# Kernel optimization log

Measured on AMD Instinct MI355X. Metric: run time of the kernel, lower is better.

## Reference

```python
import jax, jax.numpy as jnp
from jax import lax
import numpy as np

VTH = 0.2
DECAY = 0.25            # LIF membrane decay used by pcdmd slayers.LIFSpike (STBP-style)
DT = 0.001              # norse default integration step
TAU_SYN_INV = 200.0     # norse LSNNParameters defaults
TAU_MEM_INV = 100.0
TAU_ADAPT_INV = 1.0 / 700.0
BETA = 0.0              # module sets beta=0 (no threshold adaptation jumps)
ALPHA = 100.0           # SuperSpike surrogate slope (norse 'super' method)

@jax.custom_vjp
def spike_rect(v):
    # Heaviside forward, rectangular surrogate backward (STBP)
    return (v > 0).astype(v.dtype)

def _sr_fwd(v):
    return spike_rect(v), v

def _sr_bwd(v, g):
    return (g * (jnp.abs(v) < 0.5).astype(g.dtype),)

spike_rect.defvjp(_sr_fwd, _sr_bwd)

@jax.custom_vjp
def spike_super(v):
    # Heaviside forward, SuperSpike surrogate backward (norse 'super')
    return (v > 0).astype(v.dtype)

def _ss_fwd(v):
    return spike_super(v), v

def _ss_bwd(v, g):
    return (g / (ALPHA * jnp.abs(v) + 1.0) ** 2,)

spike_super.defvjp(_ss_fwd, _ss_bwd)

def lif_spike(x):
    # x: [..., T] -> spike train [..., T]
    # u_t = DECAY * u_{t-1} * (1 - o_{t-1}) + x_t ; o_t = H(u_t - VTH)
    xT = jnp.moveaxis(x, -1, 0)  # [T, ...]
    u0 = jnp.zeros(xT.shape[1:], x.dtype)
    def step(carry, xt):
        u, o = carry
        u = DECAY * u * (1.0 - o) + xt
        o = spike_rect(u - VTH)
        return (u, o), o
    _, out = lax.scan(step, (u0, u0), xT)
    return jnp.moveaxis(out, 0, -1)

def lsnn_recurrent(x, w_in, w_rec):
    # x: [T, B, H] input spikes; norse LSNNRecurrent lsnn_step with beta=0, v_th=VTH
    x_in = jnp.einsum('tbh,oh->tbo', x, w_in)  # input current, hoisted out of scan
    B, H = x.shape[1], w_in.shape[0]
    z0 = jnp.zeros((B, H), x.dtype)
    state0 = (z0, z0, z0, jnp.full((B, H), VTH, x.dtype))  # z, v, i, b (b starts at v_th)
    def step(state, xt):
        z, v, i, b = state
        i_jump = i + xt + z @ w_rec.T
        v_dec = v + DT * TAU_MEM_INV * (-v + i_jump)          # v_leak = 0
        i_dec = i_jump - DT * TAU_SYN_INV * i_jump
        b_dec = b + DT * TAU_ADAPT_INV * (VTH - b)
        z_new = spike_super(v_dec - b_dec)
        v_new = (1.0 - z_new) * v_dec                          # v_reset = 0
        b_new = b_dec + z_new * TAU_ADAPT_INV * BETA
        return (z_new, v_new, i_dec, b_new), z_new
    _, out = lax.scan(step, state0, x_in)
    return out  # [T, B, H]

def setup_inputs() -> dict:
    key = jax.random.key(0)
    ks = jax.random.split(key, 7)
    B, T = 64, 8192
    EEG_C, AUD_C, H, OUT = 64, 1, 10, 2
    x = jax.random.normal(ks[0], (B, 1, EEG_C + 2 * AUD_C, T), jnp.float32)
    s_in = 1.0 / float(np.sqrt(EEG_C))
    s_h = 1.0 / float(np.sqrt(H))
    return {
        'x': x,
        'w_front': jax.random.uniform(ks[1], (H, EEG_C), jnp.float32, -s_in, s_in),
        'b_front': jax.random.uniform(ks[2], (H,), jnp.float32, -s_in, s_in),
        'w_in': jax.random.uniform(ks[3], (H, H), jnp.float32, -s_h, s_h),
        'w_rec': jax.random.uniform(ks[4], (H, H), jnp.float32, -s_h, s_h),
        'w_cls': jax.random.uniform(ks[5], (OUT, H), jnp.float32, -s_h, s_h),
        'b_cls': jax.random.uniform(ks[6], (OUT,), jnp.float32, -s_h, s_h),
    }

def reference(x, w_front, b_front, w_in, w_rec, w_cls, b_cls):
    AUD_C = 1
    window_length = x.shape[-1]
    eeg = x[:, 0, AUD_C:-AUD_C, :]                              # [B, 64, T]
    eeg = jnp.einsum('bct,hc->bht', eeg, w_front) + b_front[None, :, None]
    eeg = lif_spike(eeg)                                        # spike_tanh in snn mode
    eeg = jnp.transpose(eeg, (2, 0, 1))                         # [T, B, H]
    z = lsnn_recurrent(eeg, w_in, w_rec)                        # [T, B, H]
    out = jnp.transpose(z, (1, 2, 0))                           # [B, H, T]
    out = jnp.einsum('bht,oh->bot', out, w_cls) + b_cls[None, :, None]
    out = lif_spike(out)                                        # spike_sigmoid in snn mode
    return jnp.sum(out, axis=2) / window_length                 # [B, 2]
```

## Files before the change

### kernel.cpp

```cpp
#include <hip/hip_runtime.h>
#include <cstdint>
#include <cstddef>

#define T_LEN 8192
#define BATCH 64
#define HID   10
#define CH    66
#define EEG   64
#define SM_STRIDE 8384
#define TS    1060

__global__ __launch_bounds__(256) void k_front_lif(
    const float* __restrict__ x, const float* __restrict__ wf_g,
    const float* __restrict__ bf_g, unsigned short* __restrict__ smask,
    float* __restrict__ out) {
    __shared__ float wf[EEG][HID];
    __shared__ float bf[HID];
    __shared__ float yt[HID][TS];
    int tid = threadIdx.x;
    for (int i = tid; i < EEG * HID; i += 256) {
        int h = i / EEG, c = i % EEG;
        wf[c][h] = wf_g[i];
    }
    if (tid < HID) bf[tid] = bf_g[tid];

    int chunk = blockIdx.x;
    int b     = blockIdx.y;
    if (chunk == 0) {
        for (int i = tid; i < 96; i += 256)
            ((unsigned*)(smask + (size_t)b * SM_STRIDE))[i] = 0u;
        if (b == 0)
            for (int i = tid; i < BATCH * 2; i += 256) out[i] = 0.f;
    }
    __syncthreads();

    int t0 = chunk * 1024;
    const float* xb = x + ((size_t)b * CH + 1) * T_LEN;
    for (int g = tid; g < 264; g += 256) {
        int t = t0 - 32 + 4 * g;
        if (t < 0) continue;
        float acc[4][HID];
#pragma unroll
        for (int j = 0; j < 4; ++j)
#pragma unroll
            for (int h = 0; h < HID; ++h) acc[j][h] = bf[h];
        const float* xp = xb + t;
#pragma unroll 4
        for (int c = 0; c < EEG; ++c) {
            float4 xv = *(const float4*)(xp + (size_t)c * T_LEN);
#pragma unroll
            for (int h = 0; h < HID; ++h) {
                float w = wf[c][h];
                acc[0][h] = fmaf(xv.x, w, acc[0][h]);
                acc[1][h] = fmaf(xv.y, w, acc[1][h]);
                acc[2][h] = fmaf(xv.z, w, acc[2][h]);
                acc[3][h] = fmaf(xv.w, w, acc[3][h]);
            }
        }
        int k = 4 * g;
#pragma unroll
        for (int h = 0; h < HID; ++h)
            *(float4*)&yt[h][k] =
                make_float4(acc[0][h], acc[1][h], acc[2][h], acc[3][h]);
    }
    __syncthreads();

    int w    = tid >> 6;
    int lane = tid & 63;
    int h    = lane & 15;
    int hh   = h < HID ? h : HID - 1;

    int kliv = 32 + 256 * w;
    int wl   = (chunk == 0 && w == 0) ? 0 : 32;
    int ks   = kliv - wl;
    int nf   = (256 + wl) >> 2;
    const float4* yrow = (const float4*)&yt[hh][0];
    int base = ks >> 2;

    unsigned short* smb = smask + (size_t)b * SM_STRIDE + 192 + t0 + 256 * w;
    float u = 0.f, o = 0.f;
    float4 A = yrow[base], B = yrow[base + 1];
    for (int f = 0; f < nf; ++f) {
        int nx = f + 2; if (nx > nf - 1) nx = nf - 1;
        float4 C = yrow[base + nx];
        float vv[4] = {A.x, A.y, A.z, A.w};
        int kb = ks + 4 * f;
#pragma unroll
        for (int k2 = 0; k2 < 4; ++k2) {
            u = (o > 0.5f) ? vv[k2] : fmaf(0.25f, u, vv[k2]);
            bool sp = (u > 0.2f);
            o = sp ? 1.0f : 0.0f;
            unsigned long long bal = __ballot(sp);
            int k = kb + k2;
            if (k >= kliv && h == 0)
                smb[k - kliv] = (unsigned short)(bal & 0x3FFull);
        }
        A = B; B = C;
    }
}

__global__ __launch_bounds__(512) void k_lsnn(
    const unsigned short* __restrict__ smask,
    const float* __restrict__ w_in, const float* __restrict__ w_rec,
    const float* __restrict__ w_cls, const float* __restrict__ b_cls,
    float* __restrict__ out) {
    extern __shared__ float LDSBUF[];
    float* T = LDSBUF;
    float* D = LDSBUF + 1536;
    int tid = threadIdx.x;
    for (int i = tid; i < 1536; i += 512) {
        int hi = i / 768;
        int rem = i - hi * 768;
        int m = rem / 24, role = rem - m * 24;
        float s = 0.f;
        if (role < 22) {
            const float* wrow = (role < 10) ? (w_in + role * HID)
                              : (role < 12) ? (w_cls + (role - 10) * HID)
                                            : (w_rec + (role - 12) * HID);
#pragma unroll
            for (int j = 0; j < 5; ++j)
                if (m & (1u << j)) s += wrow[hi * 5 + j];
        }
        T[i] = s;
    }
    __syncthreads();
    for (int i = tid; i < 1024 * 22; i += 512) {
        int z = i / 22, role = i - z * 22;
        D[i] = T[(z & 31) * 24 + role] + T[768 + (z >> 5) * 24 + role];
    }
    __syncthreads();

    int lane = tid & 63;
    int q = lane >> 4;
    int r = lane & 15;
    int rr = r < 12 ? r : 11;
    int rrec = 12 + (r < HID ? r : 9);
    int shq = q * 16;
    int id = blockIdx.x * 32 + (tid >> 4);
    int b = id >> 7, chunk = id & 127;

    float bcl = (r == 10 || r == 11) ? b_cls[r - HID] : 0.f;

    const unsigned short* sm = smask + (size_t)b * SM_STRIDE + (size_t)chunk * 64;

    auto xlook = [&](const uint4& mv, float* X) {
        unsigned hw[8] = { mv.x & 0x3FFu, (mv.x >> 16) & 0x3FFu,
                           mv.y & 0x3FFu, (mv.y >> 16) & 0x3FFu,
                           mv.z & 0x3FFu, (mv.z >> 16) & 0x3FFu,
                           mv.w & 0x3FFu, (mv.w >> 16) & 0x3FFu };
#pragma unroll
        for (int u = 0; u < 8; ++u)
            X[u] = D[hw[u] * 22 + rr];
    };

    uint4 mB = *(const uint4*)(sm + 8);
    uint4 mC = *(const uint4*)(sm + 16);
    uint4 mD = *(const uint4*)(sm + 24);
    float Xc[8], Xn[8], Pc[8], Pn[8];
    { uint4 m0 = *(const uint4*)(sm); xlook(m0, Xc); }
#pragma unroll
    for (int u = 0; u < 8; ++u) { Pc[u] = 0.f; Pn[u] = 0.f; }

    float v = 0.f, cur = 0.f;
    unsigned zmask = 0;
    float uc = 0.f, oc = 0.f, accs = 0.f;

    for (int gr = 0; gr < 32; ++gr) {
        int nb = gr + 4; if (nb > 31) nb = 31;
        uint4 mE = *(const uint4*)(sm + (size_t)nb * 8);
        xlook(mB, Xn);
        unsigned zs[8];
#pragma unroll
        for (int u = 0; u < 8; ++u) {
            float rec = D[zmask * 22 + rrec];
            float ij = (cur + Xc[u]) + rec;
            float vd = v + 0.1f * (ij - v);
            cur = ij - 0.2f * ij;
            bool zb = vd > 0.2f;
            unsigned long long bal = __ballot(zb);
            v = zb ? 0.f : vd;
            zmask = (unsigned)(bal >> shq) & 0x3FFu;
            zs[u] = zmask;
        }
        if (gr >= 21) {
#pragma unroll
            for (int u = 0; u < 8; ++u)
                Pn[u] = D[zs[u] * 22 + rr];
        }
        if (gr >= 22) {
            bool in = (gr >= 25);
#pragma unroll
            for (int u = 0; u < 8; ++u) {
                float ci = Pc[u] + bcl;
                uc = (oc > 0.5f) ? ci : fmaf(0.25f, uc, ci);
                oc = (uc > 0.2f) ? 1.f : 0.f;
                if (in) accs += oc;
            }
        }
#pragma unroll
        for (int u = 0; u < 8; ++u) { Xc[u] = Xn[u]; Pc[u] = Pn[u]; }
        mB = mC; mC = mD; mD = mE;
    }
#pragma unroll
    for (int u = 0; u < 8; ++u) {
        float ci = Pc[u] + bcl;
        uc = (oc > 0.5f) ? ci : fmaf(0.25f, uc, ci);
        oc = (uc > 0.2f) ? 1.f : 0.f;
        accs += oc;
    }
    if (r == 10 || r == 11)
        atomicAdd(&out[b * 2 + (r - 10)], accs * (1.0f / 8192.0f));
}

extern "C" void kernel_launch(void* const* d_in, const int* in_sizes, int n_in,
                              void* d_out, int out_size, void* d_ws, size_t ws_size,
                              hipStream_t stream) {
    const float* x       = (const float*)d_in[0];
    const float* w_front = (const float*)d_in[1];
    const float* b_front = (const float*)d_in[2];
    const float* w_in    = (const float*)d_in[3];
    const float* w_rec   = (const float*)d_in[4];
    const float* w_cls   = (const float*)d_in[5];
    const float* b_cls   = (const float*)d_in[6];
    float* out = (float*)d_out;

    unsigned short* smask = (unsigned short*)d_ws;

    k_front_lif<<<dim3(8, BATCH), 256, 0, stream>>>(x, w_front, b_front, smask, out);
    k_lsnn<<<dim3(256), 512, (1536 + 1024 * 22) * sizeof(float), stream>>>(
        smask, w_in, w_rec, w_cls, b_cls, out);
}
```

Baseline: 277.6 us.

## Halve front-end chunk size, double grid, and software-pipeline channel loads

The front projection+LIF kernel now processes 512-sample chunks over a 16x64 grid instead of 1024-sample chunks over 8x64, so more blocks run and each wave's serial LIF scan covers 128 steps instead of 256. Each thread now computes two time steps with float2 loads, prefetches 8 channels ahead in a register ring, and reads padded weights as vector LDS loads. The LIF scan prefetches one more float4 ahead. The trade-off is that the 32-step warm-up overlap is recomputed for twice as many chunks, which adds redundant projection and scan work.

```diff
diff --git a/kernel.cpp b/kernel.cpp
--- a/kernel.cpp
+++ b/kernel.cpp
@@ -8,19 +8,20 @@
 #define CH    66
 #define EEG   64
 #define SM_STRIDE 8384
-#define TS    1060
+#define CHK   512
+#define TS2   548
 
 __global__ __launch_bounds__(256) void k_front_lif(
     const float* __restrict__ x, const float* __restrict__ wf_g,
     const float* __restrict__ bf_g, unsigned short* __restrict__ smask,
     float* __restrict__ out) {
-    __shared__ float wf[EEG][HID];
+    __shared__ float wf[EEG][12];
     __shared__ float bf[HID];
-    __shared__ float yt[HID][TS];
+    __shared__ float yt[HID][TS2];
     int tid = threadIdx.x;
-    for (int i = tid; i < EEG * HID; i += 256) {
-        int h = i / EEG, c = i % EEG;
-        wf[c][h] = wf_g[i];
+    for (int i = tid; i < EEG * 12; i += 256) {
+        int c = i / 12, h = i - 12 * (i / 12);
+        wf[c][h] = (h < HID) ? wf_g[h * EEG + c] : 0.f;
     }
     if (tid < HID) bf[tid] = bf_g[tid];
 
@@ -34,34 +35,41 @@
     }
     __syncthreads();
 
-    int t0 = chunk * 1024;
+    int t0 = chunk * CHK;
     const float* xb = x + ((size_t)b * CH + 1) * T_LEN;
-    for (int g = tid; g < 264; g += 256) {
-        int t = t0 - 32 + 4 * g;
+    for (int g = tid; g < 272; g += 256) {
+        int t = t0 - 32 + 2 * g;
         if (t < 0) continue;
-        float acc[4][HID];
-#pragma unroll
-        for (int j = 0; j < 4; ++j)
-#pragma unroll
-            for (int h = 0; h < HID; ++h) acc[j][h] = bf[h];
         const float* xp = xb + t;
-#pragma unroll 4
+        float2 xv[8];
+#pragma unroll
+        for (int c = 0; c < 8; ++c) xv[c] = *(const float2*)(xp + (size_t)c * T_LEN);
+        float a0[HID], a1[HID];
+#pragma unroll
+        for (int h = 0; h < HID; ++h) { a0[h] = bf[h]; a1[h] = bf[h]; }
+#pragma unroll
         for (int c = 0; c < EEG; ++c) {
-            float4 xv = *(const float4*)(xp + (size_t)c * T_LEN);
-#pragma unroll
-            for (int h = 0; h < HID; ++h) {
-                float w = wf[c][h];
-                acc[0][h] = fmaf(xv.x, w, acc[0][h]);
-                acc[1][h] = fmaf(xv.y, w, acc[1][h]);
-                acc[2][h] = fmaf(xv.z, w, acc[2][h]);
-                acc[3][h] = fmaf(xv.w, w, acc[3][h]);
-            }
-        }
-        int k = 4 * g;
+            float2 xc = xv[c & 7];
+            if (c + 8 < EEG)
+                xv[c & 7] = *(const float2*)(xp + (size_t)(c + 8) * T_LEN);
+            float4 w0 = *(const float4*)&wf[c][0];
+            float4 w1 = *(const float4*)&wf[c][4];
+            float2 w2 = *(const float2*)&wf[c][8];
+            a0[0] = fmaf(xc.x, w0.x, a0[0]);  a1[0] = fmaf(xc.y, w0.x, a1[0]);
+            a0[1] = fmaf(xc.x, w0.y, a0[1]);  a1[1] = fmaf(xc.y, w0.y, a1[1]);
+            a0[2] = fmaf(xc.x, w0.z, a0[2]);  a1[2] = fmaf(xc.y, w0.z, a1[2]);
+            a0[3] = fmaf(xc.x, w0.w, a0[3]);  a1[3] = fmaf(xc.y, w0.w, a1[3]);
+            a0[4] = fmaf(xc.x, w1.x, a0[4]);  a1[4] = fmaf(xc.y, w1.x, a1[4]);
+            a0[5] = fmaf(xc.x, w1.y, a0[5]);  a1[5] = fmaf(xc.y, w1.y, a1[5]);
+            a0[6] = fmaf(xc.x, w1.z, a0[6]);  a1[6] = fmaf(xc.y, w1.z, a1[6]);
+            a0[7] = fmaf(xc.x, w1.w, a0[7]);  a1[7] = fmaf(xc.y, w1.w, a1[7]);
+            a0[8] = fmaf(xc.x, w2.x, a0[8]);  a1[8] = fmaf(xc.y, w2.x, a1[8]);
+            a0[9] = fmaf(xc.x, w2.y, a0[9]);  a1[9] = fmaf(xc.y, w2.y, a1[9]);
+        }
+        int k = 2 * g;
 #pragma unroll
         for (int h = 0; h < HID; ++h)
-            *(float4*)&yt[h][k] =
-                make_float4(acc[0][h], acc[1][h], acc[2][h], acc[3][h]);
+            *(float2*)&yt[h][k] = make_float2(a0[h], a1[h]);
     }
     __syncthreads();
 
@@ -70,19 +78,19 @@
     int h    = lane & 15;
     int hh   = h < HID ? h : HID - 1;
 
-    int kliv = 32 + 256 * w;
+    int kliv = 32 + 128 * w;
     int wl   = (chunk == 0 && w == 0) ? 0 : 32;
     int ks   = kliv - wl;
-    int nf   = (256 + wl) >> 2;
+    int nf   = (128 + wl) >> 2;
     const float4* yrow = (const float4*)&yt[hh][0];
     int base = ks >> 2;
 
-    unsigned short* smb = smask + (size_t)b * SM_STRIDE + 192 + t0 + 256 * w;
+    unsigned short* smb = smask + (size_t)b * SM_STRIDE + 192 + t0 + 128 * w;
     float u = 0.f, o = 0.f;
-    float4 A = yrow[base], B = yrow[base + 1];
+    float4 A = yrow[base], B = yrow[base + 1], C = yrow[base + 2];
     for (int f = 0; f < nf; ++f) {
-        int nx = f + 2; if (nx > nf - 1) nx = nf - 1;
-        float4 C = yrow[base + nx];
+        int nx = f + 3; if (nx > nf - 1) nx = nf - 1;
+        float4 D = yrow[base + nx];
         float vv[4] = {A.x, A.y, A.z, A.w};
         int kb = ks + 4 * f;
 #pragma unroll
@@ -95,7 +103,7 @@
             if (k >= kliv && h == 0)
                 smb[k - kliv] = (unsigned short)(bal & 0x3FFull);
         }
-        A = B; B = C;
+        A = B; B = C; C = D;
     }
 }
 
@@ -226,7 +234,7 @@
 
     unsigned short* smask = (unsigned short*)d_ws;
 
-    k_front_lif<<<dim3(8, BATCH), 256, 0, stream>>>(x, w_front, b_front, smask, out);
+    k_front_lif<<<dim3(16, BATCH), 256, 0, stream>>>(x, w_front, b_front, smask, out);
     k_lsnn<<<dim3(256), 512, (1536 + 1024 * 22) * sizeof(float), stream>>>(
         smask, w_in, w_rec, w_cls, b_cls, out);
 }
```

Measured after the change: 581.8 us. 110% more time.
